# Kernel tuning notes

Measured on AMD Instinct MI355X. Metric: run time of the kernel, lower is better.

The kernel has to match this reference:

```python
import jax, jax.numpy as jnp
import numpy as np

B, T, C, H = 4096, 32, 180, 6
HD = C // H  # 30
EPS = 1e-5

def _ln(x, g, b):
    mu = jnp.mean(x, axis=-1, keepdims=True)
    var = jnp.mean(jnp.square(x - mu), axis=-1, keepdims=True)
    return (x - mu) * jax.lax.rsqrt(var + EPS) * g + b

def setup_inputs() -> dict:
    key = jax.random.key(0)
    ks = jax.random.split(key, 12)
    s_in = 1.0 / np.sqrt(C)
    s_ff = 1.0 / np.sqrt(4 * C)
    return {
        "x": jax.random.normal(ks[0], (B, T, C), jnp.float32),
        "wq": jax.random.normal(ks[1], (H, C, HD), jnp.float32) * s_in,
        "wk": jax.random.normal(ks[2], (H, C, HD), jnp.float32) * s_in,
        "wv": jax.random.normal(ks[3], (H, C, HD), jnp.float32) * s_in,
        "g1": jnp.ones((C,), jnp.float32),
        "be1": jnp.zeros((C,), jnp.float32),
        "g2": jnp.ones((C,), jnp.float32),
        "be2": jnp.zeros((C,), jnp.float32),
        "w1": jax.random.normal(ks[4], (C, 4 * C), jnp.float32) * s_in,
        "b1": jnp.zeros((4 * C,), jnp.float32),
        "w2": jax.random.normal(ks[5], (4 * C, C), jnp.float32) * s_ff,
        "b2": jnp.zeros((C,), jnp.float32),
    }

def reference(x, wq, wk, wv, g1, be1, g2, be2, w1, b1, w2, b2):
    Bv, Tv, Cv = x.shape
    h = _ln(x, g1, be1)
    # batched multi-head QKV (replaces per-head Python loop)
    q = jnp.einsum('btc,hcd->bhtd', h, wq)
    k = jnp.einsum('btc,hcd->bhtd', h, wk)
    v = jnp.einsum('btc,hcd->bhtd', h, wv)
    scores = jnp.einsum('bhtd,bhsd->bhts', q, k) * (HD ** -0.5)
    mask = jnp.tril(jnp.ones((Tv, Tv), bool))
    scores = jnp.where(mask, scores, -jnp.inf)
    attn = jax.nn.softmax(scores, axis=-1)  # dropout off (eval)
    out = jnp.einsum('bhts,bhsd->bhtd', attn, v)
    out = jnp.transpose(out, (0, 2, 1, 3)).reshape(Bv, Tv, Cv)  # concat heads
    x = x + out
    h2 = _ln(x, g2, be2)
    mlp = jax.nn.relu(h2 @ w1 + b1) @ w2 + b2  # dropout off (eval)
    return x + mlp
```

## Files before the change

### kernel.cpp

```cpp
#include <hip/hip_runtime.h>

typedef __attribute__((ext_vector_type(8))) short short8;
typedef __attribute__((ext_vector_type(4))) float f32x4;
typedef unsigned short ushort_t;
typedef unsigned int u32;
typedef unsigned long long u64;

#define MFMA16(a,b,c) __builtin_amdgcn_mfma_f32_16x16x32_bf16((a),(b),(c),0,0,0)
#define SBAR() __builtin_amdgcn_sched_barrier(0)

__device__ __forceinline__ ushort_t f2bf(float f){
  union { float f; u32 u; } v; v.f = f;
  u32 r = v.u + 0x7fffu + ((v.u >> 16) & 1u);
  return (ushort_t)(r >> 16);
}
__device__ __forceinline__ float bf2f(ushort_t h){
  union { u32 u; float f; } v; v.u = ((u32)h) << 16; return v.f;
}
__device__ __forceinline__ u64 pack4(float a, float b, float c, float d){
  u32 p0 = (u32)f2bf(a) | ((u32)f2bf(b) << 16);
  u32 p1 = (u32)f2bf(c) | ((u32)f2bf(d) << 16);
  return (u64)p0 | ((u64)p1 << 32);
}
__device__ __forceinline__ u32 pack2(float a, float b){
  return (u32)f2bf(a) | ((u32)f2bf(b) << 16);
}
__device__ __forceinline__ void pin(short8 &v){ asm volatile("" : "+v"(v)); }

template<int CTRL>
__device__ __forceinline__ float dpp_add(float x){
  union { float f; int i; } a, b;
  a.f = x;
  b.i = __builtin_amdgcn_update_dpp(a.i, a.i, CTRL, 0xF, 0xF, false);
  return x + b.f;
}
__device__ __forceinline__ float red4_add(float x){
  x = dpp_add<0xB1>(x); x = dpp_add<0x4E>(x);
  return x;
}

#define WQKV_ELEMS (576*192)
#define W1T_ELEMS  (768*192)
#define W2T_ELEMS  (192*768)

#define SH 200
#define SS 40
#define SA 184

__global__ void prep_weights(const float* __restrict__ wq, const float* __restrict__ wk,
                             const float* __restrict__ wv, const float* __restrict__ w1,
                             const float* __restrict__ w2, ushort_t* __restrict__ ws){
  __shared__ float lds_f[11700];
  ushort_t* wqkv = ws;
  ushort_t* w1t = ws + WQKV_ELEMS;
  ushort_t* w2t = w1t + W1T_ELEMS;
  int bid = blockIdx.x, tid = threadIdx.x;

  if (bid < 18){
    int h = bid / 3, m = bid % 3;
    const float* src = ((m == 0) ? wq : (m == 1) ? wk : wv) + (size_t)h*180*30;
    for (int l = 0; l < 22; l++){
      int idx = tid + l*256;
      if (idx < 5400) lds_f[idx] = src[idx];
    }
    __syncthreads();
    u32* dst = (u32*)wqkv;
    #pragma unroll
    for (int l = 0; l < 12; l++){
      int j = tid + l*256;
      int d = j / 96, kp = j - d*96;
      int k0 = 2*kp;
      float f0 = (d < 30 && k0   < 180) ? lds_f[k0*30 + d]     : 0.f;
      float f1 = (d < 30 && k0+1 < 180) ? lds_f[(k0+1)*30 + d] : 0.f;
      dst[(size_t)(h*96 + m*32 + d)*96 + kp] = pack2(f0, f1);
    }
  } else if (bid < 30){
    int n0 = (bid - 18) * 64;
    #pragma unroll
    for (int l = 0; l < 45; l++){
      int idx = tid + l*256;
      int c = idx >> 6, nl = idx & 63;
      int n = n0 + nl;
      lds_f[nl*180 + c] = (n < 720) ? w1[(size_t)c*720 + n] : 0.f;
    }
    __syncthreads();
    u32* dst = (u32*)w1t;
    #pragma unroll
    for (int l = 0; l < 24; l++){
      int j = tid + l*256;
      int nl = j / 96, cp = j - nl*96;
      int c0 = 2*cp;
      float f0 = (c0   < 180) ? lds_f[nl*180 + c0]     : 0.f;
      float f1 = (c0+1 < 180) ? lds_f[nl*180 + c0 + 1] : 0.f;
      dst[(size_t)(n0 + nl)*96 + cp] = pack2(f0, f1);
    }
  } else {
    int c40 = (bid - 30) * 64;
    #pragma unroll
    for (int l = 0; l < 45; l++){
      int idx = tid + l*256;
      int c4l = idx / 180, no = idx - c4l*180;
      lds_f[no*65 + c4l] = (c40 + c4l < 720) ? w2[(size_t)(c40 + c4l)*180 + no] : 0.f;
    }
    __syncthreads();
    u32* dst = (u32*)w2t;
    #pragma unroll
    for (int l = 0; l < 24; l++){
      int j = tid + l*256;
      int no = j >> 5, cp = j & 31;
      float f0 = (no < 180) ? lds_f[no*65 + 2*cp]     : 0.f;
      float f1 = (no < 180) ? lds_f[no*65 + 2*cp + 1] : 0.f;
      dst[(size_t)no*384 + (c40 >> 1) + cp] = pack2(f0, f1);
    }
  }
}

__global__ __launch_bounds__(256, 2)
void block_kernel(const float* __restrict__ x,
                  const float* __restrict__ g1, const float* __restrict__ be1,
                  const float* __restrict__ g2, const float* __restrict__ be2,
                  const float* __restrict__ b1, const float* __restrict__ b2,
                  const ushort_t* __restrict__ wqkv, const ushort_t* __restrict__ w1t,
                  const ushort_t* __restrict__ w2t, float* __restrict__ out){
  __shared__ __align__(16) ushort_t W[64*SH];
  __shared__ __align__(16) ushort_t hn[64*SH];
  __shared__ __align__(16) ushort_t att[64*SA];

  int tid = threadIdx.x;
  int wave = tid >> 6, lane = tid & 63;
  int quad = lane >> 4, c16 = lane & 15;
  long base = (long)blockIdx.x * 11520;

  {
    int row = tid >> 2, sub = tid & 3;
    int c0 = sub*48;
    f32x4 xv[12];
    #pragma unroll
    for (int gi = 0; gi < 12; gi++){
      int c = c0 + gi*4;
      if (c < 180) xv[gi] = *(const f32x4*)(x + base + (long)row*180 + c);
      else         xv[gi] = (f32x4)0.f;
    }
    SBAR();
    float s1 = 0.f, s2 = 0.f;
    #pragma unroll
    for (int gi = 0; gi < 12; gi++){
      s1 += xv[gi].x + xv[gi].y + xv[gi].z + xv[gi].w;
      s2 += xv[gi].x*xv[gi].x + xv[gi].y*xv[gi].y + xv[gi].z*xv[gi].z + xv[gi].w*xv[gi].w;
    }
    s1 = red4_add(s1); s2 = red4_add(s2);
    float mu = s1 * (1.f/180.f);
    float rstd = rsqrtf(s2 * (1.f/180.f) - mu*mu + 1e-5f);
    #pragma unroll
    for (int gi = 0; gi < 12; gi++){
      int c = c0 + gi*4;
      if (c < 180){
        f32x4 gg = *(const f32x4*)(g1 + c);
        f32x4 bb = *(const f32x4*)(be1 + c);
        *(u64*)(hn + row*SH + c) = pack4((xv[gi].x - mu)*rstd*gg.x + bb.x,
                                         (xv[gi].y - mu)*rstd*gg.y + bb.y,
                                         (xv[gi].z - mu)*rstd*gg.z + bb.z,
                                         (xv[gi].w - mu)*rstd*gg.w + bb.w);
      } else {
        *(u64*)(hn + row*SH + c) = 0ull;
      }
    }
  }
  __syncthreads();

  {
    ushort_t* buf0 = W + wave*(2*32*SS);
    ushort_t* buf1 = buf0 + 32*SS;
    const float scl = 0.18257418583505537f;

    for (int jj = 0; jj < 3; jj++){
      int j = wave*3 + jj;
      int bb = (j >= 6) ? 1 : 0;
      int head = j - 6*bb;
      const ushort_t* wbase = wqkv + head*(96*192);

      f32x4 accq[2][2], acck[2][2], accv[2][2];
      #pragma unroll
      for (int i = 0; i < 2; i++)
        #pragma unroll
        for (int jx = 0; jx < 2; jx++){ accq[i][jx]=(f32x4)0.f; acck[i][jx]=(f32x4)0.f; accv[i][jx]=(f32x4)0.f; }

      short8 aqw[2][6], akw[2][6];
      #pragma unroll
      for (int mt = 0; mt < 2; mt++)
        #pragma unroll
        for (int kk = 0; kk < 6; kk++){
          aqw[mt][kk] = *(const short8*)(wbase + (      mt*16 + c16)*192 + kk*32 + quad*8);
          akw[mt][kk] = *(const short8*)(wbase + (32  + mt*16 + c16)*192 + kk*32 + quad*8);
          pin(aqw[mt][kk]); pin(akw[mt][kk]);
        }
      SBAR();
      short8 avc[2], avn[2];
      #pragma unroll
      for (int mt = 0; mt < 2; mt++)
        avc[mt] = *(const short8*)(wbase + (64 + mt*16 + c16)*192 + quad*8);
      #pragma unroll
      for (int kk = 0; kk < 6; kk++){
        if (kk < 5){
          #pragma unroll
          for (int mt = 0; mt < 2; mt++)
            avn[mt] = *(const short8*)(wbase + (64 + mt*16 + c16)*192 + (kk+1)*32 + quad*8);
        }
        short8 hf[2];
        #pragma unroll
        for (int nt = 0; nt < 2; nt++)
          hf[nt] = *(const short8*)(hn + (bb*32 + nt*16 + c16)*SH + kk*32 + quad*8);
        #pragma unroll
        for (int mt = 0; mt < 2; mt++)
          #pragma unroll
          for (int nt = 0; nt < 2; nt++){
            accq[mt][nt] = MFMA16(aqw[mt][kk], hf[nt], accq[mt][nt]);
            acck[mt][nt] = MFMA16(akw[mt][kk], hf[nt], acck[mt][nt]);
            accv[mt][nt] = MFMA16(hf[mt], avc[nt], accv[mt][nt]);
          }
        if (kk < 5){
          #pragma unroll
          for (int mt = 0; mt < 2; mt++) avc[mt] = avn[mt];
        }
      }
      #pragma unroll
      for (int mt = 0; mt < 2; mt++)
        #pragma unroll
        for (int nt = 0; nt < 2; nt++){
          *(u64*)(buf0 + (nt*16 + c16)*SS + mt*16 + quad*4) =
            pack4(accq[mt][nt][0], accq[mt][nt][1], accq[mt][nt][2], accq[mt][nt][3]);
          *(u64*)(buf1 + (nt*16 + c16)*SS + mt*16 + quad*4) =
            pack4(acck[mt][nt][0], acck[mt][nt][1], acck[mt][nt][2], acck[mt][nt][3]);
        }
      f32x4 sacc[2][2];
      #pragma unroll
      for (int i = 0; i < 2; i++){ sacc[i][0]=(f32x4)0.f; sacc[i][1]=(f32x4)0.f; }
      short8 akf[2], bqf[2];
      #pragma unroll
      for (int mt = 0; mt < 2; mt++) akf[mt] = *(const short8*)(buf1 + (mt*16 + c16)*SS + quad*8);
      #pragma unroll
      for (int nt = 0; nt < 2; nt++) bqf[nt] = *(const short8*)(buf0 + (nt*16 + c16)*SS + quad*8);
      #pragma unroll
      for (int mt = 0; mt < 2; mt++)
        #pragma unroll
        for (int nt = 0; nt < 2; nt++)
          sacc[mt][nt] = MFMA16(akf[mt], bqf[nt], sacc[mt][nt]);
      #pragma unroll
      for (int nt = 0; nt < 2; nt++){
        int t = nt*16 + c16;
        float v[8];
        #pragma unroll
        for (int r = 0; r < 4; r++){
          int s0 = quad*4 + r, s1v = 16 + quad*4 + r;
          v[r]   = (s0  > t) ? -1e30f : sacc[0][nt][r]*scl;
          v[4+r] = (s1v > t) ? -1e30f : sacc[1][nt][r]*scl;
        }
        float m = v[0];
        #pragma unroll
        for (int i = 1; i < 8; i++) m = fmaxf(m, v[i]);
        m = fmaxf(m, __shfl_xor(m, 16));
        m = fmaxf(m, __shfl_xor(m, 32));
        float e[8], s = 0.f;
        #pragma unroll
        for (int i = 0; i < 8; i++){ e[i] = __expf(v[i] - m); s += e[i]; }
        s += __shfl_xor(s, 16);
        s += __shfl_xor(s, 32);
        float inv = 1.f / s;
        *(u64*)(buf1 + t*SS +      quad*4) = pack4(e[0]*inv, e[1]*inv, e[2]*inv, e[3]*inv);
        *(u64*)(buf1 + t*SS + 16 + quad*4) = pack4(e[4]*inv, e[5]*inv, e[6]*inv, e[7]*inv);
      }
      #pragma unroll
      for (int mt = 0; mt < 2; mt++)
        #pragma unroll
        for (int nt = 0; nt < 2; nt++)
          *(u64*)(buf0 + (nt*16 + c16)*SS + mt*16 + quad*4) =
            pack4(accv[mt][nt][0], accv[mt][nt][1], accv[mt][nt][2], accv[mt][nt][3]);
      f32x4 oacc[2][2];
      #pragma unroll
      for (int i = 0; i < 2; i++){ oacc[i][0]=(f32x4)0.f; oacc[i][1]=(f32x4)0.f; }
      short8 avf[2], bpf[2];
      #pragma unroll
      for (int mt = 0; mt < 2; mt++) avf[mt] = *(const short8*)(buf0 + (mt*16 + c16)*SS + quad*8);
      #pragma unroll
      for (int nt = 0; nt < 2; nt++) bpf[nt] = *(const short8*)(buf1 + (nt*16 + c16)*SS + quad*8);
      #pragma unroll
      for (int mt = 0; mt < 2; mt++)
        #pragma unroll
        for (int nt = 0; nt < 2; nt++)
          oacc[mt][nt] = MFMA16(avf[mt], bpf[nt], oacc[mt][nt]);
      #pragma unroll
      for (int mt = 0; mt < 2; mt++)
        #pragma unroll
        for (int nt = 0; nt < 2; nt++){
          int t = bb*32 + nt*16 + c16;
          int c = head*30 + mt*16 + quad*4;
          ushort_t* p = att + t*SA + c;
          *(u32*)(p) = pack2(oacc[mt][nt][0], oacc[mt][nt][1]);
          if (mt == 0 || quad < 3)
            *(u32*)(p + 2) = pack2(oacc[mt][nt][2], oacc[mt][nt][3]);
        }
    }
  }
  __syncthreads();

  {
    f32x4 xv2[12];
    #pragma unroll
    for (int it = 0; it < 12; it++){
      int idx = it*256 + tid;
      if (idx < 2880) xv2[it] = *(const f32x4*)(x + base + (long)idx*4);
    }
    SBAR();
    #pragma unroll
    for (int it = 0; it < 12; it++){
      int idx = it*256 + tid;
      if (idx < 2880){
        f32x4 v = xv2[it];
        int row = (int)(((u32)idx * 745655u) >> 25);
        int col4 = (idx - row*45)*4;
        u64 m = *(const u64*)(att + row*SA + col4);
        v.x += bf2f((ushort_t)(m      ));
        v.y += bf2f((ushort_t)(m >> 16));
        v.z += bf2f((ushort_t)(m >> 32));
        v.w += bf2f((ushort_t)(m >> 48));
        *(f32x4*)(out + base + (long)idx*4) = v;
        *(u64*)(hn + row*SH + col4) = pack4(v.x, v.y, v.z, v.w);
      } else {
        int p = idx - 2880;
        int row = (p*21846) >> 16;
        int g = p - row*3;
        *(u64*)(hn + row*SH + 180 + g*4) = 0ull;
      }
    }
  }
  __syncthreads();

  {
    int row = tid >> 2, sub = tid & 3;
    int c0 = sub*48;
    float s1 = 0.f, s2 = 0.f;
    u64 mv[12];
    #pragma unroll
    for (int gi = 0; gi < 12; gi++){
      mv[gi] = *(const u64*)(hn + row*SH + c0 + gi*4);
      #pragma unroll
      for (int e = 0; e < 4; e++){
        float v = bf2f((ushort_t)(mv[gi] >> (16*e)));
        s1 += v; s2 += v*v;
      }
    }
    s1 = red4_add(s1); s2 = red4_add(s2);
    float mu = s1 * (1.f/180.f);
    float rstd = rsqrtf(s2 * (1.f/180.f) - mu*mu + 1e-5f);
    #pragma unroll
    for (int gi = 0; gi < 12; gi++){
      int c = c0 + gi*4;
      if (c < 180){
        f32x4 gg = *(const f32x4*)(g2 + c);
        f32x4 bb = *(const f32x4*)(be2 + c);
        float v0 = (bf2f((ushort_t)(mv[gi]    )) - mu)*rstd*gg.x + bb.x;
        float v1 = (bf2f((ushort_t)(mv[gi]>>16)) - mu)*rstd*gg.y + bb.y;
        float v2 = (bf2f((ushort_t)(mv[gi]>>32)) - mu)*rstd*gg.z + bb.z;
        float v3 = (bf2f((ushort_t)(mv[gi]>>48)) - mu)*rstd*gg.w + bb.w;
        *(u64*)(hn + row*SH + c) = pack4(v0, v1, v2, v3);
      }
    }
  }
  __syncthreads();

  {
    ushort_t* act = W;
    f32x4 outacc[4][3];
    #pragma unroll
    for (int i = 0; i < 4; i++)
      #pragma unroll
      for (int jx = 0; jx < 3; jx++) outacc[i][jx] = (f32x4)0.f;

    for (int ch = 0; ch < 4; ch++){
      f32x4 aacc[3][4];
      #pragma unroll
      for (int i = 0; i < 3; i++)
        #pragma unroll
        for (int jx = 0; jx < 4; jx++) aacc[i][jx] = (f32x4)0.f;
      short8 aw[3][6];
      #pragma unroll
      for (int mi = 0; mi < 3; mi++)
        #pragma unroll
        for (int kk = 0; kk < 6; kk++){
          aw[mi][kk] = *(const short8*)(w1t + (size_t)(ch*192 + (wave*3+mi)*16 + c16)*192 + kk*32 + quad*8);
          pin(aw[mi][kk]);
        }
      SBAR();
      #pragma unroll
      for (int kk = 0; kk < 6; kk++){
        short8 bh[4];
        #pragma unroll
        for (int tt = 0; tt < 4; tt++)
          bh[tt] = *(const short8*)(hn + (tt*16 + c16)*SH + kk*32 + quad*8);
        #pragma unroll
        for (int mi = 0; mi < 3; mi++)
          #pragma unroll
          for (int tt = 0; tt < 4; tt++)
            aacc[mi][tt] = MFMA16(aw[mi][kk], bh[tt], aacc[mi][tt]);
      }
      __syncthreads();
      #pragma unroll
      for (int mi = 0; mi < 3; mi++){
        int nrel = (wave*3+mi)*16 + quad*4;
        int nabs = ch*192 + nrel;
        f32x4 bias = (f32x4)0.f;
        if (nabs < 720) bias = *(const f32x4*)(b1 + nabs);
        #pragma unroll
        for (int tt = 0; tt < 4; tt++){
          float v0 = fmaxf(aacc[mi][tt][0] + bias[0], 0.f);
          float v1 = fmaxf(aacc[mi][tt][1] + bias[1], 0.f);
          float v2 = fmaxf(aacc[mi][tt][2] + bias[2], 0.f);
          float v3 = fmaxf(aacc[mi][tt][3] + bias[3], 0.f);
          *(u64*)(act + (tt*16 + c16)*SH + nrel) = pack4(v0, v1, v2, v3);
        }
      }
      __syncthreads();
      short8 bw[3][6];
      #pragma unroll
      for (int ntl = 0; ntl < 3; ntl++)
        #pragma unroll
        for (int kk = 0; kk < 6; kk++){
          bw[ntl][kk] = *(const short8*)(w2t + (size_t)(wave*48 + ntl*16 + c16)*768 + ch*192 + kk*32 + quad*8);
          pin(bw[ntl][kk]);
        }
      SBAR();
      #pragma unroll
      for (int kk = 0; kk < 6; kk++){
        short8 aa[4];
        #pragma unroll
        for (int tt = 0; tt < 4; tt++)
          aa[tt] = *(const short8*)(act + (tt*16 + c16)*SH + kk*32 + quad*8);
        #pragma unroll
        for (int tt = 0; tt < 4; tt++)
          #pragma unroll
          for (int ntl = 0; ntl < 3; ntl++)
            outacc[tt][ntl] = MFMA16(aa[tt], bw[ntl][kk], outacc[tt][ntl]);
      }
    }
    #pragma unroll
    for (int ntl = 0; ntl < 3; ntl++){
      int no = wave*48 + ntl*16 + c16;
      if (no < 180){
        float bias = b2[no];
        #pragma unroll
        for (int tt = 0; tt < 4; tt++){
          #pragma unroll
          for (int r = 0; r < 4; r++){
            long a = base + (long)(tt*16 + quad*4 + r)*180 + no;
            out[a] = out[a] + outacc[tt][ntl][r] + bias;
          }
        }
      }
    }
  }
}

extern "C" void kernel_launch(void* const* d_in, const int* in_sizes, int n_in,
                              void* d_out, int out_size, void* d_ws, size_t ws_size,
                              hipStream_t stream) {
  const float* x   = (const float*)d_in[0];
  const float* wq  = (const float*)d_in[1];
  const float* wk  = (const float*)d_in[2];
  const float* wv  = (const float*)d_in[3];
  const float* g1  = (const float*)d_in[4];
  const float* be1 = (const float*)d_in[5];
  const float* g2  = (const float*)d_in[6];
  const float* be2 = (const float*)d_in[7];
  const float* w1  = (const float*)d_in[8];
  const float* b1  = (const float*)d_in[9];
  const float* w2  = (const float*)d_in[10];
  const float* b2  = (const float*)d_in[11];
  ushort_t* ws   = (ushort_t*)d_ws;
  ushort_t* wqkv = ws;
  ushort_t* w1t  = ws + WQKV_ELEMS;
  ushort_t* w2t  = w1t + W1T_ELEMS;
  float* out = (float*)d_out;

  prep_weights<<<42, 256, 0, stream>>>(wq, wk, wv, w1, w2, ws);
  block_kernel<<<2048, 256, 0, stream>>>(x, g1, be1, g2, be2, b1, b2,
                                         wqkv, w1t, w2t, out);
}
```

Before: 516.0 us.

## Drop register-pinned weight prefetch and stream weights per k-step in rolled loops

```diff
diff --git a/kernel.cpp b/kernel.cpp
--- a/kernel.cpp
+++ b/kernel.cpp
@@ -7,7 +7,6 @@
 typedef unsigned long long u64;
 
 #define MFMA16(a,b,c) __builtin_amdgcn_mfma_f32_16x16x32_bf16((a),(b),(c),0,0,0)
-#define SBAR() __builtin_amdgcn_sched_barrier(0)
 
 __device__ __forceinline__ ushort_t f2bf(float f){
   union { float f; u32 u; } v; v.f = f;
@@ -25,7 +24,6 @@
 __device__ __forceinline__ u32 pack2(float a, float b){
   return (u32)f2bf(a) | ((u32)f2bf(b) << 16);
 }
-__device__ __forceinline__ void pin(short8 &v){ asm volatile("" : "+v"(v)); }
 
 template<int CTRL>
 __device__ __forceinline__ float dpp_add(float x){
@@ -65,7 +63,6 @@
     }
     __syncthreads();
     u32* dst = (u32*)wqkv;
-    #pragma unroll
     for (int l = 0; l < 12; l++){
       int j = tid + l*256;
       int d = j / 96, kp = j - d*96;
@@ -76,7 +73,6 @@
     }
   } else if (bid < 30){
     int n0 = (bid - 18) * 64;
-    #pragma unroll
     for (int l = 0; l < 45; l++){
       int idx = tid + l*256;
       int c = idx >> 6, nl = idx & 63;
@@ -85,7 +81,6 @@
     }
     __syncthreads();
     u32* dst = (u32*)w1t;
-    #pragma unroll
     for (int l = 0; l < 24; l++){
       int j = tid + l*256;
       int nl = j / 96, cp = j - nl*96;
@@ -96,7 +91,6 @@
     }
   } else {
     int c40 = (bid - 30) * 64;
-    #pragma unroll
     for (int l = 0; l < 45; l++){
       int idx = tid + l*256;
       int c4l = idx / 180, no = idx - c4l*180;
@@ -104,7 +98,6 @@
     }
     __syncthreads();
     u32* dst = (u32*)w2t;
-    #pragma unroll
     for (int l = 0; l < 24; l++){
       int j = tid + l*256;
       int no = j >> 5, cp = j & 31;
@@ -131,22 +124,36 @@
   int quad = lane >> 4, c16 = lane & 15;
   long base = (long)blockIdx.x * 11520;
 
+  #pragma unroll 1
+  for (int it = 0; it < 12; it++){
+    int idx = it*256 + tid;
+    if (idx < 2880){
+      f32x4 v = *(const f32x4*)(x + base + (long)idx*4);
+      int row = (int)(((u32)idx * 745655u) >> 25);
+      int col = idx - row*45;
+      *(u64*)(hn + row*SH + col*4) = pack4(v.x, v.y, v.z, v.w);
+    } else {
+      int p = idx - 2880;
+      int row = (p*21846) >> 16;
+      int g = p - row*3;
+      *(u64*)(hn + row*SH + 180 + g*4) = 0ull;
+    }
+  }
+  __syncthreads();
+
   {
     int row = tid >> 2, sub = tid & 3;
     int c0 = sub*48;
-    f32x4 xv[12];
+    float s1 = 0.f, s2 = 0.f;
+    u64 mv[12];
     #pragma unroll
     for (int gi = 0; gi < 12; gi++){
-      int c = c0 + gi*4;
-      if (c < 180) xv[gi] = *(const f32x4*)(x + base + (long)row*180 + c);
-      else         xv[gi] = (f32x4)0.f;
-    }
-    SBAR();
-    float s1 = 0.f, s2 = 0.f;
-    #pragma unroll
-    for (int gi = 0; gi < 12; gi++){
-      s1 += xv[gi].x + xv[gi].y + xv[gi].z + xv[gi].w;
-      s2 += xv[gi].x*xv[gi].x + xv[gi].y*xv[gi].y + xv[gi].z*xv[gi].z + xv[gi].w*xv[gi].w;
+      mv[gi] = *(const u64*)(hn + row*SH + c0 + gi*4);
+      #pragma unroll
+      for (int e = 0; e < 4; e++){
+        float v = bf2f((ushort_t)(mv[gi] >> (16*e)));
+        s1 += v; s2 += v*v;
+      }
     }
     s1 = red4_add(s1); s2 = red4_add(s2);
     float mu = s1 * (1.f/180.f);
@@ -157,12 +164,11 @@
       if (c < 180){
         f32x4 gg = *(const f32x4*)(g1 + c);
         f32x4 bb = *(const f32x4*)(be1 + c);
-        *(u64*)(hn + row*SH + c) = pack4((xv[gi].x - mu)*rstd*gg.x + bb.x,
-                                         (xv[gi].y - mu)*rstd*gg.y + bb.y,
-                                         (xv[gi].z - mu)*rstd*gg.z + bb.z,
-                                         (xv[gi].w - mu)*rstd*gg.w + bb.w);
-      } else {
-        *(u64*)(hn + row*SH + c) = 0ull;
+        float v0 = (bf2f((ushort_t)(mv[gi]    )) - mu)*rstd*gg.x + bb.x;
+        float v1 = (bf2f((ushort_t)(mv[gi]>>16)) - mu)*rstd*gg.y + bb.y;
+        float v2 = (bf2f((ushort_t)(mv[gi]>>32)) - mu)*rstd*gg.z + bb.z;
+        float v3 = (bf2f((ushort_t)(mv[gi]>>48)) - mu)*rstd*gg.w + bb.w;
+        *(u64*)(hn + row*SH + c) = pack4(v0, v1, v2, v3);
       }
     }
   }
@@ -173,6 +179,7 @@
     ushort_t* buf1 = buf0 + 32*SS;
     const float scl = 0.18257418583505537f;
 
+    #pragma unroll 1
     for (int jj = 0; jj < 3; jj++){
       int j = wave*3 + jj;
       int bb = (j >= 6) ? 1 : 0;
@@ -185,43 +192,30 @@
         #pragma unroll
         for (int jx = 0; jx < 2; jx++){ accq[i][jx]=(f32x4)0.f; acck[i][jx]=(f32x4)0.f; accv[i][jx]=(f32x4)0.f; }
 
-      short8 aqw[2][6], akw[2][6];
-      #pragma unroll
-      for (int mt = 0; mt < 2; mt++)
-        #pragma unroll
-        for (int kk = 0; kk < 6; kk++){
-          aqw[mt][kk] = *(const short8*)(wbase + (      mt*16 + c16)*192 + kk*32 + quad*8);
-          akw[mt][kk] = *(const short8*)(wbase + (32  + mt*16 + c16)*192 + kk*32 + quad*8);
-          pin(aqw[mt][kk]); pin(akw[mt][kk]);
-        }
-      SBAR();
-      short8 avc[2], avn[2];
-      #pragma unroll
-      for (int mt = 0; mt < 2; mt++)
-        avc[mt] = *(const short8*)(wbase + (64 + mt*16 + c16)*192 + quad*8);
-      #pragma unroll
+      #pragma unroll 1
       for (int kk = 0; kk < 6; kk++){
-        if (kk < 5){
-          #pragma unroll
-          for (int mt = 0; mt < 2; mt++)
-            avn[mt] = *(const short8*)(wbase + (64 + mt*16 + c16)*192 + (kk+1)*32 + quad*8);
-        }
-        short8 hf[2];
-        #pragma unroll
-        for (int nt = 0; nt < 2; nt++)
-          hf[nt] = *(const short8*)(hn + (bb*32 + nt*16 + c16)*SH + kk*32 + quad*8);
-        #pragma unroll
-        for (int mt = 0; mt < 2; mt++)
-          #pragma unroll
-          for (int nt = 0; nt < 2; nt++){
-            accq[mt][nt] = MFMA16(aqw[mt][kk], hf[nt], accq[mt][nt]);
-            acck[mt][nt] = MFMA16(akw[mt][kk], hf[nt], acck[mt][nt]);
-            accv[mt][nt] = MFMA16(hf[mt], avc[nt], accv[mt][nt]);
-          }
-        if (kk < 5){
-          #pragma unroll
-          for (int mt = 0; mt < 2; mt++) avc[mt] = avn[mt];
-        }
+        const ushort_t* wk0 = wbase + c16*192 + kk*32 + quad*8;
+        short8 aq0 = *(const short8*)(wk0);
+        short8 aq1 = *(const short8*)(wk0 + 16*192);
+        short8 ak0 = *(const short8*)(wk0 + 32*192);
+        short8 ak1 = *(const short8*)(wk0 + 48*192);
+        short8 av0 = *(const short8*)(wk0 + 64*192);
+        short8 av1 = *(const short8*)(wk0 + 80*192);
+        const ushort_t* hb = hn + (bb*32 + c16)*SH + kk*32 + quad*8;
+        short8 hf0 = *(const short8*)(hb);
+        short8 hf1 = *(const short8*)(hb + 16*SH);
+        accq[0][0] = MFMA16(aq0, hf0, accq[0][0]);
+        accq[0][1] = MFMA16(aq0, hf1, accq[0][1]);
+        accq[1][0] = MFMA16(aq1, hf0, accq[1][0]);
+        accq[1][1] = MFMA16(aq1, hf1, accq[1][1]);
+        acck[0][0] = MFMA16(ak0, hf0, acck[0][0]);
+        acck[0][1] = MFMA16(ak0, hf1, acck[0][1]);
+        acck[1][0] = MFMA16(ak1, hf0, acck[1][0]);
+        acck[1][1] = MFMA16(ak1, hf1, acck[1][1]);
+        accv[0][0] = MFMA16(hf0, av0, accv[0][0]);
+        accv[0][1] = MFMA16(hf0, av1, accv[0][1]);
+        accv[1][0] = MFMA16(hf1, av0, accv[1][0]);
+        accv[1][1] = MFMA16(hf1, av1, accv[1][1]);
       }
       #pragma unroll
       for (int mt = 0; mt < 2; mt++)
@@ -303,34 +297,20 @@
   }
   __syncthreads();
 
-  {
-    f32x4 xv2[12];
-    #pragma unroll
-    for (int it = 0; it < 12; it++){
-      int idx = it*256 + tid;
-      if (idx < 2880) xv2[it] = *(const f32x4*)(x + base + (long)idx*4);
-    }
-    SBAR();
-    #pragma unroll
-    for (int it = 0; it < 12; it++){
-      int idx = it*256 + tid;
-      if (idx < 2880){
-        f32x4 v = xv2[it];
-        int row = (int)(((u32)idx * 745655u) >> 25);
-        int col4 = (idx - row*45)*4;
-        u64 m = *(const u64*)(att + row*SA + col4);
-        v.x += bf2f((ushort_t)(m      ));
-        v.y += bf2f((ushort_t)(m >> 16));
-        v.z += bf2f((ushort_t)(m >> 32));
-        v.w += bf2f((ushort_t)(m >> 48));
-        *(f32x4*)(out + base + (long)idx*4) = v;
-        *(u64*)(hn + row*SH + col4) = pack4(v.x, v.y, v.z, v.w);
-      } else {
-        int p = idx - 2880;
-        int row = (p*21846) >> 16;
-        int g = p - row*3;
-        *(u64*)(hn + row*SH + 180 + g*4) = 0ull;
-      }
+  #pragma unroll 1
+  for (int it = 0; it < 12; it++){
+    int idx = it*256 + tid;
+    if (idx < 2880){
+      f32x4 v = *(const f32x4*)(x + base + (long)idx*4);
+      int row = (int)(((u32)idx * 745655u) >> 25);
+      int col4 = (idx - row*45)*4;
+      u64 m = *(const u64*)(att + row*SA + col4);
+      v.x += bf2f((ushort_t)(m      ));
+      v.y += bf2f((ushort_t)(m >> 16));
+      v.z += bf2f((ushort_t)(m >> 32));
+      v.w += bf2f((ushort_t)(m >> 48));
+      *(f32x4*)(out + base + (long)idx*4) = v;
+      *(u64*)(hn + row*SH + col4) = pack4(v.x, v.y, v.z, v.w);
     }
   }
   __syncthreads();
@@ -376,32 +356,36 @@
       #pragma unroll
       for (int jx = 0; jx < 3; jx++) outacc[i][jx] = (f32x4)0.f;
 
+    #pragma unroll 1
     for (int ch = 0; ch < 4; ch++){
       f32x4 aacc[3][4];
       #pragma unroll
       for (int i = 0; i < 3; i++)
         #pragma unroll
         for (int jx = 0; jx < 4; jx++) aacc[i][jx] = (f32x4)0.f;
-      short8 aw[3][6];
-      #pragma unroll
-      for (int mi = 0; mi < 3; mi++)
-        #pragma unroll
-        for (int kk = 0; kk < 6; kk++){
-          aw[mi][kk] = *(const short8*)(w1t + (size_t)(ch*192 + (wave*3+mi)*16 + c16)*192 + kk*32 + quad*8);
-          pin(aw[mi][kk]);
-        }
-      SBAR();
-      #pragma unroll
+      #pragma unroll 1
       for (int kk = 0; kk < 6; kk++){
-        short8 bh[4];
-        #pragma unroll
-        for (int tt = 0; tt < 4; tt++)
-          bh[tt] = *(const short8*)(hn + (tt*16 + c16)*SH + kk*32 + quad*8);
-        #pragma unroll
-        for (int mi = 0; mi < 3; mi++)
-          #pragma unroll
-          for (int tt = 0; tt < 4; tt++)
-            aacc[mi][tt] = MFMA16(aw[mi][kk], bh[tt], aacc[mi][tt]);
+        const ushort_t* wb = w1t + (size_t)(ch*192 + wave*48 + c16)*192 + kk*32 + quad*8;
+        short8 aw0 = *(const short8*)(wb);
+        short8 aw1 = *(const short8*)(wb + 16*192);
+        short8 aw2 = *(const short8*)(wb + 32*192);
+        const ushort_t* hb = hn + c16*SH + kk*32 + quad*8;
+        short8 bh0 = *(const short8*)(hb);
+        short8 bh1 = *(const short8*)(hb + 16*SH);
+        short8 bh2 = *(const short8*)(hb + 32*SH);
+        short8 bh3 = *(const short8*)(hb + 48*SH);
+        aacc[0][0] = MFMA16(aw0, bh0, aacc[0][0]);
+        aacc[0][1] = MFMA16(aw0, bh1, aacc[0][1]);
+        aacc[0][2] = MFMA16(aw0, bh2, aacc[0][2]);
+        aacc[0][3] = MFMA16(aw0, bh3, aacc[0][3]);
+        aacc[1][0] = MFMA16(aw1, bh0, aacc[1][0]);
+        aacc[1][1] = MFMA16(aw1, bh1, aacc[1][1]);
+        aacc[1][2] = MFMA16(aw1, bh2, aacc[1][2]);
+        aacc[1][3] = MFMA16(aw1, bh3, aacc[1][3]);
+        aacc[2][0] = MFMA16(aw2, bh0, aacc[2][0]);
+        aacc[2][1] = MFMA16(aw2, bh1, aacc[2][1]);
+        aacc[2][2] = MFMA16(aw2, bh2, aacc[2][2]);
+        aacc[2][3] = MFMA16(aw2, bh3, aacc[2][3]);
       }
       __syncthreads();
       #pragma unroll
@@ -420,26 +404,29 @@
         }
       }
       __syncthreads();
-      short8 bw[3][6];
-      #pragma unroll
-      for (int ntl = 0; ntl < 3; ntl++)
-        #pragma unroll
-        for (int kk = 0; kk < 6; kk++){
-          bw[ntl][kk] = *(const short8*)(w2t + (size_t)(wave*48 + ntl*16 + c16)*768 + ch*192 + kk*32 + quad*8);
-          pin(bw[ntl][kk]);
-        }
-      SBAR();
-      #pragma unroll
+      #pragma unroll 1
       for (int kk = 0; kk < 6; kk++){
-        short8 aa[4];
-        #pragma unroll
-        for (int tt = 0; tt < 4; tt++)
-          aa[tt] = *(const short8*)(act + (tt*16 + c16)*SH + kk*32 + quad*8);
-        #pragma unroll
-        for (int tt = 0; tt < 4; tt++)
-          #pragma unroll
-          for (int ntl = 0; ntl < 3; ntl++)
-            outacc[tt][ntl] = MFMA16(aa[tt], bw[ntl][kk], outacc[tt][ntl]);
+        const ushort_t* wb = w2t + (size_t)(wave*48 + c16)*768 + ch*192 + kk*32 + quad*8;
+        short8 bw0 = *(const short8*)(wb);
+        short8 bw1 = *(const short8*)(wb + 16*768);
+        short8 bw2 = *(const short8*)(wb + 32*768);
+        const ushort_t* ab = act + c16*SH + kk*32 + quad*8;
+        short8 aa0 = *(const short8*)(ab);
+        short8 aa1 = *(const short8*)(ab + 16*SH);
+        short8 aa2 = *(const short8*)(ab + 32*SH);
+        short8 aa3 = *(const short8*)(ab + 48*SH);
+        outacc[0][0] = MFMA16(aa0, bw0, outacc[0][0]);
+        outacc[0][1] = MFMA16(aa0, bw1, outacc[0][1]);
+        outacc[0][2] = MFMA16(aa0, bw2, outacc[0][2]);
+        outacc[1][0] = MFMA16(aa1, bw0, outacc[1][0]);
+        outacc[1][1] = MFMA16(aa1, bw1, outacc[1][1]);
+        outacc[1][2] = MFMA16(aa1, bw2, outacc[1][2]);
+        outacc[2][0] = MFMA16(aa2, bw0, outacc[2][0]);
+        outacc[2][1] = MFMA16(aa2, bw1, outacc[2][1]);
+        outacc[2][2] = MFMA16(aa2, bw2, outacc[2][2]);
+        outacc[3][0] = MFMA16(aa3, bw0, outacc[3][0]);
+        outacc[3][1] = MFMA16(aa3, bw1, outacc[3][1]);
+        outacc[3][2] = MFMA16(aa3, bw2, outacc[3][2]);
       }
     }
     #pragma unroll
```

Result: no change. 513.8 us (-0.4%).
